# Kernel optimization log

Hardware: AMD Instinct MI355X
Metric: run time of the kernel (lower is better)

The kernel has to match this reference:

```python
import jax, jax.numpy as jnp
import numpy as np

B, T, D = 2, 2048, 1024
H, HS = 16, 64  # n_head, head_size; H*HS == D
THETA = 10000.0


def setup_inputs() -> dict:
    key = jax.random.key(0)
    ks = jax.random.split(key, 10)
    s = 0.02
    return {
        "x": jax.random.normal(ks[0], (B, T, D), jnp.float32),
        "attention_mask": jnp.ones((B, T), jnp.int32),
        # weights stored [in, out] (transposed torch Linear weight)
        "Wq": jax.random.normal(ks[1], (D, H * HS), jnp.float32) * s,
        "bq": jax.random.normal(ks[2], (H * HS,), jnp.float32) * s,
        "Wk": jax.random.normal(ks[3], (D, H * HS), jnp.float32) * s,
        "bk": jax.random.normal(ks[4], (H * HS,), jnp.float32) * s,
        "Wv": jax.random.normal(ks[5], (D, H * HS), jnp.float32) * s,
        "bv": jax.random.normal(ks[6], (H * HS,), jnp.float32) * s,
        "Wo": jax.random.normal(ks[7], (H * HS, D), jnp.float32) * s,
        "bo": jax.random.normal(ks[8], (D,), jnp.float32) * s,
    }


def _rotate_half(x):
    x1, x2 = x[..., : HS // 2], x[..., HS // 2:]
    return jnp.concatenate((-x2, x1), axis=-1)


def _rope_tables(seq_len, dtype):
    inv_freq = 1.0 / (THETA ** (jnp.arange(0, HS, 2, dtype=jnp.float32) / HS))
    t = jnp.arange(seq_len, dtype=jnp.float32)
    freqs = t[:, None] * inv_freq[None, :]            # [T, HS/2]
    emb = jnp.concatenate((freqs, freqs), axis=-1)    # [T, HS]
    return jnp.cos(emb).astype(dtype), jnp.sin(emb).astype(dtype)


def attention_fwd(x, attention_mask, Wq, bq, Wk, bk, Wv, bv, Wo, bo):
    b, t, c = x.shape
    # QKV projections -> [B, H, T, HS]
    q = (x @ Wq + bq).reshape(b, t, H, HS).transpose(0, 2, 1, 3)
    k = (x @ Wk + bk).reshape(b, t, H, HS).transpose(0, 2, 1, 3)
    v = (x @ Wv + bv).reshape(b, t, H, HS).transpose(0, 2, 1, 3)
    # rotary embedding
    cos, sin = _rope_tables(t, x.dtype)               # [T, HS]
    q = q * cos + _rotate_half(q) * sin
    k = k * cos + _rotate_half(k) * sin
    # expanded causal+padding mask: mask[:,None,None,:] expanded to [B,1,T,T] then tril
    causal = jnp.tril(jnp.ones((t, t), dtype=bool))
    keep = (attention_mask[:, None, None, :] != 0) & causal[None, None]  # [B,1,T,T]
    scale = 1.0 / np.sqrt(HS)
    scores = jnp.einsum('bhqd,bhkd->bhqk', q, k) * scale
    scores = jnp.where(keep, scores, jnp.finfo(scores.dtype).min)
    att = jax.nn.softmax(scores, axis=-1)
    y = jnp.einsum('bhqk,bhkd->bhqd', att, v)         # [B,H,T,HS]
    y = y.transpose(0, 2, 1, 3).reshape(b, t, H * HS)
    return y @ Wo + bo


def reference(x, attention_mask, Wq, bq, Wk, bk, Wv, bv, Wo, bo):
    return attention_fwd(x, attention_mask, Wq, bq, Wk, bk, Wv, bv, Wo, bo)
```

## Files before the change

kernel.cpp:

```cpp
#include <hip/hip_runtime.h>

#define T_SEQ 2048
#define NB 2
#define NH 16
#define HS 64
#define DMODEL 1024
#define NEG_BIG (-3.0e38f)
#define FIXED_M 16.0f

typedef __attribute__((ext_vector_type(8))) short bf16x8;
typedef __attribute__((ext_vector_type(4))) float f32x4;
#define MFMA16 __builtin_amdgcn_mfma_f32_16x16x32_bf16

__device__ __forceinline__ float bfu2f(unsigned int u) {
    union { unsigned int i; float f; } z; z.i = u << 16; return z.f;
}
__device__ __forceinline__ unsigned short f2bfu(float f) {
    union { float f; unsigned int i; } z; z.f = f;
    unsigned int x = z.i;
    unsigned int r = x + 0x7fffu + ((x >> 16) & 1u);
    return (unsigned short)(r >> 16);
}
__device__ __forceinline__ unsigned int pack_bf16(float a, float b) {
    union { float f; unsigned int u; } x, y; x.f = a; y.f = b;
    return __builtin_amdgcn_perm(y.u + 0x8000u, x.u + 0x8000u, 0x07060302u);
}
__device__ __forceinline__ void gl2lds16(const unsigned short* g, unsigned short* l) {
    __builtin_amdgcn_global_load_lds(
        (const __attribute__((address_space(1))) unsigned int*)g,
        (__attribute__((address_space(3))) unsigned int*)l, 16, 0, 0);
}

__global__ __launch_bounds__(256) void prep_kernel(
    const float4* __restrict__ x4, ushort4* __restrict__ o4,
    const float* __restrict__ W0, const float* __restrict__ W1,
    const float* __restrict__ W2, const float* __restrict__ W3,
    unsigned short* __restrict__ T0, unsigned short* __restrict__ T1,
    unsigned short* __restrict__ T2, unsigned short* __restrict__ T3)
{
    const int t = threadIdx.x;
    if (blockIdx.z < 4) {
        __shared__ float tile[32][33];
        const float* W = (blockIdx.z == 0) ? W0 : (blockIdx.z == 1) ? W1 : (blockIdx.z == 2) ? W2 : W3;
        unsigned short* T = (blockIdx.z == 0) ? T0 : (blockIdx.z == 1) ? T1 : (blockIdx.z == 2) ? T2 : T3;
        const int k0 = blockIdx.x * 32, n0 = blockIdx.y * 32;
        const int r = t >> 5, c = t & 31;
        #pragma unroll
        for (int i = 0; i < 4; ++i)
            tile[r + 8 * i][c] = W[(size_t)(k0 + r + 8 * i) * DMODEL + n0 + c];
        __syncthreads();
        #pragma unroll
        for (int i = 0; i < 4; ++i)
            T[(size_t)(n0 + r + 8 * i) * DMODEL + k0 + c] = f2bfu(tile[c][r + 8 * i]);
    } else {
        const int n4 = NB * T_SEQ * DMODEL / 4;
        for (int i = (blockIdx.y * 32 + blockIdx.x) * 256 + t; i < n4; i += 32 * 32 * 256) {
            float4 f = x4[i];
            ushort4 u;
            u.x = f2bfu(f.x); u.y = f2bfu(f.y); u.z = f2bfu(f.z); u.w = f2bfu(f.w);
            o4[i] = u;
        }
    }
}

__global__ __launch_bounds__(256) void qkv_mfma_kernel(
    const unsigned short* __restrict__ A,
    const unsigned short* __restrict__ Wqt, const unsigned short* __restrict__ Wkt,
    const unsigned short* __restrict__ Wvt,
    const float* __restrict__ bq, const float* __restrict__ bk, const float* __restrict__ bv,
    unsigned short* __restrict__ qo, unsigned short* __restrict__ ko,
    unsigned short* __restrict__ vt)
{
    __shared__ unsigned short As[64 * 64];
    __shared__ unsigned short Bs[128 * 64];
    const int tid = threadIdx.x;
    const int wave = tid >> 6, lane = tid & 63;
    const int lane15 = lane & 15, quad = lane >> 4;
    const int sw = lane15 & 7;
    const int z = blockIdx.z;
    const unsigned short* Bt = (z == 0) ? Wqt : (z == 1) ? Wkt : Wvt;
    const float* bias = (z == 0) ? bq : (z == 1) ? bk : bv;
    const int m0 = blockIdx.x * 64, n0 = blockIdx.y * 128;
    const int mh = (wave & 1) * 32, nh = (wave >> 1) * 64;
    const int oks0 = ((0 + quad) ^ sw) * 8;
    const int oks1 = ((4 + quad) ^ sw) * 8;

    f32x4 acc[2][4];
    #pragma unroll
    for (int i = 0; i < 2; ++i)
        #pragma unroll
        for (int j = 0; j < 4; ++j) acc[i][j] = (f32x4){0.f, 0.f, 0.f, 0.f};

    int srow[4], soff[4];
    #pragma unroll
    for (int it = 0; it < 4; ++it) {
        int cc = it * 256 + tid;
        srow[it] = cc >> 3;
        soff[it] = ((cc & 7) ^ (srow[it] & 7)) * 8;
    }

    for (int kk = 0; kk < 16; ++kk) {
        __syncthreads();
        #pragma unroll
        for (int it = 0; it < 2; ++it) {
            int cc = it * 256 + tid;
            gl2lds16(A + (size_t)(m0 + srow[it]) * DMODEL + kk * 64 + soff[it], As + cc * 8);
        }
        #pragma unroll
        for (int it = 0; it < 4; ++it) {
            int cc = it * 256 + tid;
            gl2lds16(Bt + (size_t)(n0 + srow[it]) * DMODEL + kk * 64 + soff[it], Bs + cc * 8);
        }
        __syncthreads();
        #pragma unroll
        for (int ks = 0; ks < 2; ++ks) {
            const int o = ks ? oks1 : oks0;
            bf16x8 af[2], bfr[4];
            #pragma unroll
            for (int i = 0; i < 2; ++i)
                af[i] = *(const bf16x8*)(As + (mh + i * 16 + lane15) * 64 + o);
            #pragma unroll
            for (int j = 0; j < 4; ++j)
                bfr[j] = *(const bf16x8*)(Bs + (nh + j * 16 + lane15) * 64 + o);
            #pragma unroll
            for (int i = 0; i < 2; ++i)
                #pragma unroll
                for (int j = 0; j < 4; ++j)
                    acc[i][j] = MFMA16(af[i], bfr[j], acc[i][j], 0, 0, 0);
        }
    }

    const int n0c = n0 + nh;
    const int head = n0c >> 6;
    const float bj0 = bias[n0c + lane15];
    const float bj1 = bias[n0c + 16 + lane15];
    const float bj2 = bias[n0c + 32 + lane15];
    const float bj3 = bias[n0c + 48 + lane15];

    if (z < 2) {
        unsigned short* outp = (z == 0) ? qo : ko;
        const float osc = (z == 0) ? 0.18033688011112042f : 1.0f;
        const float inv0 = __builtin_exp2f(-(float)(lane15)      * 0.41524101186092029f);
        const float inv1 = __builtin_exp2f(-(float)(lane15 + 16) * 0.41524101186092029f);
        #pragma unroll
        for (int i = 0; i < 2; ++i) {
            #pragma unroll
            for (int r = 0; r < 4; ++r) {
                int tok = m0 + mh + i * 16 + quad * 4 + r;
                int bb = tok >> 11, t = tok & (T_SEQ - 1);
                float a0 = (float)t * inv0, a1 = (float)t * inv1;
                float sn0, cs0, sn1, cs1;
                __sincosf(a0, &sn0, &cs0);
                __sincosf(a1, &sn1, &cs1);
                float v0 = acc[i][0][r] + bj0, v1 = acc[i][1][r] + bj1;
                float v2 = acc[i][2][r] + bj2, v3 = acc[i][3][r] + bj3;
                size_t base = ((size_t)(bb * NH + head) * T_SEQ + t) * HS;
                outp[base + lane15]      = f2bfu((v0 * cs0 - v2 * sn0) * osc);
                outp[base + 16 + lane15] = f2bfu((v1 * cs1 - v3 * sn1) * osc);
                outp[base + 32 + lane15] = f2bfu((v2 * cs0 + v0 * sn0) * osc);
                outp[base + 48 + lane15] = f2bfu((v3 * cs1 + v1 * sn1) * osc);
            }
        }
    } else {
        #pragma unroll
        for (int i = 0; i < 2; ++i) {
            int tok0_ = m0 + mh + i * 16 + quad * 4;
            int bb = tok0_ >> 11, t0 = tok0_ & (T_SEQ - 1);
            #pragma unroll
            for (int j = 0; j < 4; ++j) {
                float bj = (j == 0) ? bj0 : (j == 1) ? bj1 : (j == 2) ? bj2 : bj3;
                ushort4 u;
                u.x = f2bfu(acc[i][j][0] + bj);
                u.y = f2bfu(acc[i][j][1] + bj);
                u.z = f2bfu(acc[i][j][2] + bj);
                u.w = f2bfu(acc[i][j][3] + bj);
                *(ushort4*)(vt + ((size_t)(bb * NH + head) * HS + j * 16 + lane15) * T_SEQ + t0) = u;
            }
        }
    }
}

__global__ __launch_bounds__(128, 2) void attn_mfma_kernel(
    const unsigned short* __restrict__ q,
    const unsigned short* __restrict__ k,
    const unsigned short* __restrict__ vt,
    const int* __restrict__ mask,
    unsigned short* __restrict__ pO,
    float* __restrict__ pl)
{
    __shared__ unsigned short Ks[64 * 64];
    __shared__ unsigned short Vs[64 * 64];
    __shared__ unsigned short Pt[2][32 * 64];
    const int tid = threadIdx.x;
    const int wave = tid >> 6, lane = tid & 63;
    const int lane15 = lane & 15, quad = lane >> 4;
    const int sw = lane15 & 7;
    const int oks0 = ((0 + quad) ^ sw) * 8;
    const int oks1 = ((4 + quad) ^ sw) * 8;
    const int bid = blockIdx.x;
    const int bh = bid & 31;
    const int u = 79 - (bid >> 5);
    int qB, c;
    if (u < 8)       { qB = u;                 c = 0; }
    else if (u < 24) { int t = u - 8;  qB = 8  + (t >> 1); c = t & 1; }
    else if (u < 48) { int t = u - 24; qB = 16 + t / 3;    c = t % 3; }
    else             { int t = u - 48; qB = 24 + (t >> 2); c = t & 3; }
    const int slot = bh * 80 + u;
    const int nc  = (qB + 8) >> 3;
    const int len = (qB + nc) / nc;
    const int kt0 = c * len;
    const int kt1 = (kt0 + len - 1 < qB) ? kt0 + len - 1 : qB;
    const int b = bh >> 4;
    const int q0 = qB * 64 + wave * 32;

    const unsigned short* kbase = k  + (size_t)bh * T_SEQ * HS;
    const unsigned short* vbase = vt + (size_t)bh * HS * T_SEQ;

    bf16x8 qf[2][2];
    #pragma unroll
    for (int g = 0; g < 2; ++g) {
        const unsigned short* qrow = q + ((size_t)bh * T_SEQ + q0 + g * 16 + lane15) * HS;
        qf[g][0] = *(const bf16x8*)(qrow + quad * 8);
        qf[g][1] = *(const bf16x8*)(qrow + 32 + quad * 8);
    }

    f32x4 accO[2][4];
    #pragma unroll
    for (int g = 0; g < 2; ++g)
        #pragma unroll
        for (int dt = 0; dt < 4; ++dt) accO[g][dt] = (f32x4){0.f, 0.f, 0.f, 0.f};
    float l_part[2] = {0.f, 0.f};

    int srow[4], soff[4];
    #pragma unroll
    for (int it = 0; it < 4; ++it) {
        int cc = it * 128 + tid;
        srow[it] = cc >> 3;
        soff[it] = ((cc & 7) ^ (srow[it] & 7)) * 8;
    }

    for (int kt = kt0; kt <= kt1; ++kt) {
        const int k0 = kt * 64;
        __syncthreads();
        #pragma unroll
        for (int it = 0; it < 4; ++it) {
            int cc = it * 128 + tid;
            gl2lds16(kbase + (size_t)(k0 + srow[it]) * HS + soff[it], Ks + cc * 8);
            gl2lds16(vbase + (size_t)srow[it] * T_SEQ + k0 + soff[it], Vs + cc * 8);
        }
        unsigned long long bal = __ballot(mask[b * T_SEQ + k0 + lane] != 0);
        __syncthreads();

        f32x4 s[2][4];
        #pragma unroll
        for (int jt = 0; jt < 4; ++jt) {
            bf16x8 kf0 = *(const bf16x8*)(Ks + (jt * 16 + lane15) * 64 + oks0);
            bf16x8 kf1 = *(const bf16x8*)(Ks + (jt * 16 + lane15) * 64 + oks1);
            #pragma unroll
            for (int g = 0; g < 2; ++g) {
                f32x4 t_ = (f32x4){0.f, 0.f, 0.f, 0.f};
                t_ = MFMA16(kf0, qf[g][0], t_, 0, 0, 0);
                t_ = MFMA16(kf1, qf[g][1], t_, 0, 0, 0);
                s[g][jt] = t_;
            }
        }

        const bool need_mask = (k0 + 63 > q0) || (bal != ~0ull);
        if (need_mask) {
            #pragma unroll
            for (int g = 0; g < 2; ++g) {
                const int qpos = q0 + g * 16 + lane15;
                #pragma unroll
                for (int jt = 0; jt < 4; ++jt) {
                    unsigned int mnib = (unsigned int)(bal >> (jt * 16 + quad * 4)) & 15u;
                    #pragma unroll
                    for (int r = 0; r < 4; ++r) {
                        int kpos = k0 + jt * 16 + quad * 4 + r;
                        bool ok = (kpos <= qpos) && ((mnib >> r) & 1u);
                        s[g][jt][r] = ok ? s[g][jt][r] : NEG_BIG;
                    }
                }
            }
        }
        #pragma unroll
        for (int g = 0; g < 2; ++g)
            #pragma unroll
            for (int jt = 0; jt < 4; ++jt)
                #pragma unroll
                for (int r = 0; r < 4; ++r) {
                    float p = exp2f(s[g][jt][r] - FIXED_M);
                    s[g][jt][r] = p;
                    l_part[g] += p;
                }

        #pragma unroll
        for (int g = 0; g < 2; ++g)
            #pragma unroll
            for (int jt = 0; jt < 4; ++jt) {
                unsigned int p01 = pack_bf16(s[g][jt][0], s[g][jt][1]);
                unsigned int p23 = pack_bf16(s[g][jt][2], s[g][jt][3]);
                int pchunk = (2 * jt + (quad >> 1)) ^ sw;
                int paddr = (g * 16 + lane15) * 64 + pchunk * 8 + (quad & 1) * 4;
                *(uint2*)(&Pt[wave][paddr]) = make_uint2(p01, p23);
            }

        bf16x8 pf[2][2];
        #pragma unroll
        for (int g = 0; g < 2; ++g) {
            pf[g][0] = *(const bf16x8*)(&Pt[wave][(g * 16 + lane15) * 64 + oks0]);
            pf[g][1] = *(const bf16x8*)(&Pt[wave][(g * 16 + lane15) * 64 + oks1]);
        }
        #pragma unroll
        for (int dt = 0; dt < 4; ++dt) {
            bf16x8 vf0 = *(const bf16x8*)(Vs + (dt * 16 + lane15) * 64 + oks0);
            bf16x8 vf1 = *(const bf16x8*)(Vs + (dt * 16 + lane15) * 64 + oks1);
            #pragma unroll
            for (int g = 0; g < 2; ++g) {
                accO[g][dt] = MFMA16(pf[g][0], vf0, accO[g][dt], 0, 0, 0);
                accO[g][dt] = MFMA16(pf[g][1], vf1, accO[g][dt], 0, 0, 0);
            }
        }
    }

    unsigned short* ob = pO + (size_t)slot * 4096;
    #pragma unroll
    for (int g = 0; g < 2; ++g)
        #pragma unroll
        for (int r = 0; r < 4; ++r) {
            int row = wave * 32 + g * 16 + quad * 4 + r;
            #pragma unroll
            for (int dt = 0; dt < 4; ++dt)
                ob[row * 64 + dt * 16 + lane15] = f2bfu(accO[g][dt][r]);
        }
    #pragma unroll
    for (int g = 0; g < 2; ++g) {
        float l = l_part[g];
        l += __shfl_xor(l, 16);
        l += __shfl_xor(l, 32);
        if (quad == 0)
            pl[slot * 64 + wave * 32 + g * 16 + lane15] = l;
    }
}

__global__ __launch_bounds__(256) void attn_combine_kernel(
    const unsigned short* __restrict__ pO, const float* __restrict__ pl,
    unsigned short* __restrict__ y)
{
    const int qB = blockIdx.x, bh = blockIdx.y;
    const int b = bh >> 4, h = bh & 15;
    const int tid = threadIdx.x;
    const int row = tid >> 2, cb = (tid & 3) * 16;
    const int nch = (qB + 8) >> 3;
    const int p = (qB < 8) ? qB : (qB < 16) ? 8 + 2 * (qB - 8)
               : (qB < 24) ? 24 + 3 * (qB - 16) : 48 + 4 * (qB - 24);
    const int slot0 = bh * 80 + p;

    float L = 0.f;
    for (int ch = 0; ch < nch; ++ch) L += pl[(slot0 + ch) * 64 + row];
    const float invL = 1.0f / L;

    float a[16];
    #pragma unroll
    for (int i = 0; i < 16; ++i) a[i] = 0.f;
    for (int ch = 0; ch < nch; ++ch) {
        const unsigned short* o = pO + (size_t)(slot0 + ch) * 4096 + row * 64 + cb;
        #pragma unroll
        for (int j = 0; j < 4; ++j) {
            ushort4 u = *(const ushort4*)(o + j * 4);
            a[j * 4 + 0] += bfu2f(u.x); a[j * 4 + 1] += bfu2f(u.y);
            a[j * 4 + 2] += bfu2f(u.z); a[j * 4 + 3] += bfu2f(u.w);
        }
    }
    unsigned short* yrow = y + (size_t)(b * T_SEQ + qB * 64 + row) * DMODEL + h * HS + cb;
    #pragma unroll
    for (int j = 0; j < 4; ++j) {
        ushort4 o;
        o.x = f2bfu(a[j * 4 + 0] * invL); o.y = f2bfu(a[j * 4 + 1] * invL);
        o.z = f2bfu(a[j * 4 + 2] * invL); o.w = f2bfu(a[j * 4 + 3] * invL);
        *(ushort4*)(yrow + j * 4) = o;
    }
}

__global__ __launch_bounds__(256) void outproj_mfma_kernel(
    const unsigned short* __restrict__ A,
    const unsigned short* __restrict__ Bt,
    const float* __restrict__ bo, float* __restrict__ out)
{
    __shared__ unsigned short As[64 * 64];
    __shared__ unsigned short Bs[128 * 64];
    const int tid = threadIdx.x;
    const int wave = tid >> 6, lane = tid & 63;
    const int lane15 = lane & 15, quad = lane >> 4;
    const int sw = lane15 & 7;
    const int oks0 = ((0 + quad) ^ sw) * 8;
    const int oks1 = ((4 + quad) ^ sw) * 8;
    const int m0 = blockIdx.x * 64, n0 = blockIdx.y * 128;
    const int mh = (wave & 1) * 32, nh = (wave >> 1) * 64;

    f32x4 acc[2][4];
    #pragma unroll
    for (int i = 0; i < 2; ++i)
        #pragma unroll
        for (int j = 0; j < 4; ++j) acc[i][j] = (f32x4){0.f, 0.f, 0.f, 0.f};

    int srow[4], soff[4];
    #pragma unroll
    for (int it = 0; it < 4; ++it) {
        int cc = it * 256 + tid;
        srow[it] = cc >> 3;
        soff[it] = ((cc & 7) ^ (srow[it] & 7)) * 8;
    }

    for (int kk = 0; kk < 16; ++kk) {
        __syncthreads();
        #pragma unroll
        for (int it = 0; it < 2; ++it) {
            int cc = it * 256 + tid;
            gl2lds16(A + (size_t)(m0 + srow[it]) * DMODEL + kk * 64 + soff[it], As + cc * 8);
        }
        #pragma unroll
        for (int it = 0; it < 4; ++it) {
            int cc = it * 256 + tid;
            gl2lds16(Bt + (size_t)(n0 + srow[it]) * DMODEL + kk * 64 + soff[it], Bs + cc * 8);
        }
        __syncthreads();
        #pragma unroll
        for (int ks = 0; ks < 2; ++ks) {
            const int o = ks ? oks1 : oks0;
            bf16x8 af[2], bfr[4];
            #pragma unroll
            for (int i = 0; i < 2; ++i)
                af[i] = *(const bf16x8*)(As + (mh + i * 16 + lane15) * 64 + o);
            #pragma unroll
            for (int j = 0; j < 4; ++j)
                bfr[j] = *(const bf16x8*)(Bs + (nh + j * 16 + lane15) * 64 + o);
            #pragma unroll
            for (int i = 0; i < 2; ++i)
                #pragma unroll
                for (int j = 0; j < 4; ++j)
                    acc[i][j] = MFMA16(af[i], bfr[j], acc[i][j], 0, 0, 0);
        }
    }

    const int n0c = n0 + nh;
    const float bj0 = bo[n0c + lane15];
    const float bj1 = bo[n0c + 16 + lane15];
    const float bj2 = bo[n0c + 32 + lane15];
    const float bj3 = bo[n0c + 48 + lane15];
    #pragma unroll
    for (int i = 0; i < 2; ++i) {
        #pragma unroll
        for (int r = 0; r < 4; ++r) {
            int tok = m0 + mh + i * 16 + quad * 4 + r;
            float* orow = out + (size_t)tok * DMODEL + n0c;
            orow[lane15]      = acc[i][0][r] + bj0;
            orow[16 + lane15] = acc[i][1][r] + bj1;
            orow[32 + lane15] = acc[i][2][r] + bj2;
            orow[48 + lane15] = acc[i][3][r] + bj3;
        }
    }
}

extern "C" void kernel_launch(void* const* d_in, const int* in_sizes, int n_in,
                              void* d_out, int out_size, void* d_ws, size_t ws_size,
                              hipStream_t stream)
{
    const float* x  = (const float*)d_in[0];
    const int* mask = (const int*)d_in[1];
    const float* Wq = (const float*)d_in[2];
    const float* bq = (const float*)d_in[3];
    const float* Wk = (const float*)d_in[4];
    const float* bk = (const float*)d_in[5];
    const float* Wv = (const float*)d_in[6];
    const float* bv = (const float*)d_in[7];
    const float* Wo = (const float*)d_in[8];
    const float* bo = (const float*)d_in[9];

    unsigned short* ws = (unsigned short*)d_ws;
    const size_t M1 = 1024 * 1024;
    unsigned short* qw  = ws;
    unsigned short* kw  = ws + 4 * M1;
    unsigned short* vtw = ws + 8 * M1;
    unsigned short* yw  = ws + 12 * M1;
    unsigned short* Wot = ws + 16 * M1;
    unsigned short* xb  = ws + 17 * M1;
    unsigned short* Wqt = ws + 21 * M1;
    unsigned short* Wkt = ws + 22 * M1;
    unsigned short* Wvt = ws + 23 * M1;
    unsigned short* pO  = ws + 17 * M1;
    float* pl = (float*)(ws + 27 * M1);

    prep_kernel<<<dim3(32, 32, 5), 256, 0, stream>>>(
        (const float4*)x, (ushort4*)xb, Wq, Wk, Wv, Wo, Wqt, Wkt, Wvt, Wot);
    qkv_mfma_kernel<<<dim3(64, 8, 3), 256, 0, stream>>>(
        xb, Wqt, Wkt, Wvt, bq, bk, bv, qw, kw, vtw);
    attn_mfma_kernel<<<2560, 128, 0, stream>>>(
        qw, kw, vtw, mask, pO, pl);
    attn_combine_kernel<<<dim3(32, 32), 256, 0, stream>>>(
        pO, pl, yw);
    outproj_mfma_kernel<<<dim3(64, 8), 256, 0, stream>>>(
        yw, Wot, bo, (float*)d_out);
}
```

Before: 188.1 us.

## Prefetch next K/V tile into registers and compute row sums with MFMA

Replaces the direct global-to-LDS async copies with a register double buffer. The next K/V tile and its mask values are loaded into registers while the current tile is computed, then written to LDS at the start of the next iteration, so global load latency overlaps with compute. The softmax denominator is now computed by an extra MFMA of the bf16 P tile against a ones vector instead of scalar adds and shuffles, and the fixed max offset subtraction before exp2 is dropped. This raises register pressure, and removing the offset risks overflow unless the scores are already offset elsewhere.

```diff
diff --git a/kernel.cpp b/kernel.cpp
--- a/kernel.cpp
+++ b/kernel.cpp
@@ -6,7 +6,6 @@
 #define HS 64
 #define DMODEL 1024
 #define NEG_BIG (-3.0e38f)
-#define FIXED_M 16.0f
 
 typedef __attribute__((ext_vector_type(8))) short bf16x8;
 typedef __attribute__((ext_vector_type(4))) float f32x4;
@@ -216,6 +215,22 @@
     const unsigned short* kbase = k  + (size_t)bh * T_SEQ * HS;
     const unsigned short* vbase = vt + (size_t)bh * HS * T_SEQ;
 
+    int srow[4], soff[4];
+    #pragma unroll
+    for (int it = 0; it < 4; ++it) {
+        int cc = it * 128 + tid;
+        srow[it] = cc >> 3;
+        soff[it] = ((cc & 7) ^ (srow[it] & 7)) * 8;
+    }
+
+    int mv = mask[b * T_SEQ + kt0 * 64 + lane];
+    uint4 kreg[4], vreg[4];
+    #pragma unroll
+    for (int it = 0; it < 4; ++it) {
+        kreg[it] = *(const uint4*)(kbase + (size_t)(kt0 * 64 + srow[it]) * HS + soff[it]);
+        vreg[it] = *(const uint4*)(vbase + (size_t)srow[it] * T_SEQ + kt0 * 64 + soff[it]);
+    }
+
     bf16x8 qf[2][2];
     #pragma unroll
     for (int g = 0; g < 2; ++g) {
@@ -224,20 +239,18 @@
         qf[g][1] = *(const bf16x8*)(qrow + 32 + quad * 8);
     }
 
+    bf16x8 ones;
+    #pragma unroll
+    for (int i = 0; i < 8; ++i) ones[i] = (short)0x3F80;
+
     f32x4 accO[2][4];
     #pragma unroll
     for (int g = 0; g < 2; ++g)
         #pragma unroll
         for (int dt = 0; dt < 4; ++dt) accO[g][dt] = (f32x4){0.f, 0.f, 0.f, 0.f};
-    float l_part[2] = {0.f, 0.f};
-
-    int srow[4], soff[4];
-    #pragma unroll
-    for (int it = 0; it < 4; ++it) {
-        int cc = it * 128 + tid;
-        srow[it] = cc >> 3;
-        soff[it] = ((cc & 7) ^ (srow[it] & 7)) * 8;
-    }
+    f32x4 acc_l[2];
+    acc_l[0] = (f32x4){0.f, 0.f, 0.f, 0.f};
+    acc_l[1] = (f32x4){0.f, 0.f, 0.f, 0.f};
 
     for (int kt = kt0; kt <= kt1; ++kt) {
         const int k0 = kt * 64;
@@ -245,10 +258,19 @@
         #pragma unroll
         for (int it = 0; it < 4; ++it) {
             int cc = it * 128 + tid;
-            gl2lds16(kbase + (size_t)(k0 + srow[it]) * HS + soff[it], Ks + cc * 8);
-            gl2lds16(vbase + (size_t)srow[it] * T_SEQ + k0 + soff[it], Vs + cc * 8);
-        }
-        unsigned long long bal = __ballot(mask[b * T_SEQ + k0 + lane] != 0);
+            *(uint4*)(Ks + cc * 8) = kreg[it];
+            *(uint4*)(Vs + cc * 8) = vreg[it];
+        }
+        unsigned long long bal = __ballot(mv != 0);
+        if (kt < kt1) {
+            const int kn = k0 + 64;
+            mv = mask[b * T_SEQ + kn + lane];
+            #pragma unroll
+            for (int it = 0; it < 4; ++it) {
+                kreg[it] = *(const uint4*)(kbase + (size_t)(kn + srow[it]) * HS + soff[it]);
+                vreg[it] = *(const uint4*)(vbase + (size_t)srow[it] * T_SEQ + kn + soff[it]);
+            }
+        }
         __syncthreads();
 
         f32x4 s[2][4];
@@ -287,11 +309,8 @@
             #pragma unroll
             for (int jt = 0; jt < 4; ++jt)
                 #pragma unroll
-                for (int r = 0; r < 4; ++r) {
-                    float p = exp2f(s[g][jt][r] - FIXED_M);
-                    s[g][jt][r] = p;
-                    l_part[g] += p;
-                }
+                for (int r = 0; r < 4; ++r)
+                    s[g][jt][r] = exp2f(s[g][jt][r]);
 
         #pragma unroll
         for (int g = 0; g < 2; ++g)
@@ -320,6 +339,11 @@
                 accO[g][dt] = MFMA16(pf[g][1], vf1, accO[g][dt], 0, 0, 0);
             }
         }
+        #pragma unroll
+        for (int g = 0; g < 2; ++g) {
+            acc_l[g] = MFMA16(pf[g][0], ones, acc_l[g], 0, 0, 0);
+            acc_l[g] = MFMA16(pf[g][1], ones, acc_l[g], 0, 0, 0);
+        }
     }
 
     unsigned short* ob = pO + (size_t)slot * 4096;
@@ -332,13 +356,12 @@
             for (int dt = 0; dt < 4; ++dt)
                 ob[row * 64 + dt * 16 + lane15] = f2bfu(accO[g][dt][r]);
         }
-    #pragma unroll
-    for (int g = 0; g < 2; ++g) {
-        float l = l_part[g];
-        l += __shfl_xor(l, 16);
-        l += __shfl_xor(l, 32);
-        if (quad == 0)
-            pl[slot * 64 + wave * 32 + g * 16 + lane15] = l;
+    if (lane15 == 0) {
+        #pragma unroll
+        for (int g = 0; g < 2; ++g)
+            #pragma unroll
+            for (int r = 0; r < 4; ++r)
+                pl[slot * 64 + wave * 32 + g * 16 + quad * 4 + r] = acc_l[g][r];
     }
 }
 
```

After: 241.5 us. 28.3% more time.

## Split attention block into four 16-row waves and compute row sums via MFMA

Applied to the files above, without the earlier changes.

The attention kernel now runs 256 threads per block, with each of four waves handling 16 query rows instead of two waves handling 32. This roughly halves per-wave register state and doubles the waves that share each K/V tile. Row sums of P are now computed with an extra MFMA against a vector of ones instead of scalar adds and shuffles. The fixed max offset of 16 is dropped from exp2, which changes numerical behaviour and could overflow for large scores. It also gives up the reuse of K/V fragments across two row groups within a wave.

```diff
diff --git a/kernel.cpp b/kernel.cpp
--- a/kernel.cpp
+++ b/kernel.cpp
@@ -6,7 +6,6 @@
 #define HS 64
 #define DMODEL 1024
 #define NEG_BIG (-3.0e38f)
-#define FIXED_M 16.0f
 
 typedef __attribute__((ext_vector_type(8))) short bf16x8;
 typedef __attribute__((ext_vector_type(4))) float f32x4;
@@ -180,7 +179,7 @@
     }
 }
 
-__global__ __launch_bounds__(128, 2) void attn_mfma_kernel(
+__global__ __launch_bounds__(256, 2) void attn_mfma_kernel(
     const unsigned short* __restrict__ q,
     const unsigned short* __restrict__ k,
     const unsigned short* __restrict__ vt,
@@ -190,7 +189,7 @@
 {
     __shared__ unsigned short Ks[64 * 64];
     __shared__ unsigned short Vs[64 * 64];
-    __shared__ unsigned short Pt[2][32 * 64];
+    __shared__ unsigned short Pt[4][16 * 64];
     const int tid = threadIdx.x;
     const int wave = tid >> 6, lane = tid & 63;
     const int lane15 = lane & 15, quad = lane >> 4;
@@ -211,30 +210,31 @@
     const int kt0 = c * len;
     const int kt1 = (kt0 + len - 1 < qB) ? kt0 + len - 1 : qB;
     const int b = bh >> 4;
-    const int q0 = qB * 64 + wave * 32;
+    const int q0w = qB * 64 + wave * 16;
 
     const unsigned short* kbase = k  + (size_t)bh * T_SEQ * HS;
     const unsigned short* vbase = vt + (size_t)bh * HS * T_SEQ;
 
-    bf16x8 qf[2][2];
-    #pragma unroll
-    for (int g = 0; g < 2; ++g) {
-        const unsigned short* qrow = q + ((size_t)bh * T_SEQ + q0 + g * 16 + lane15) * HS;
-        qf[g][0] = *(const bf16x8*)(qrow + quad * 8);
-        qf[g][1] = *(const bf16x8*)(qrow + 32 + quad * 8);
-    }
-
-    f32x4 accO[2][4];
-    #pragma unroll
-    for (int g = 0; g < 2; ++g)
-        #pragma unroll
-        for (int dt = 0; dt < 4; ++dt) accO[g][dt] = (f32x4){0.f, 0.f, 0.f, 0.f};
-    float l_part[2] = {0.f, 0.f};
-
-    int srow[4], soff[4];
-    #pragma unroll
-    for (int it = 0; it < 4; ++it) {
-        int cc = it * 128 + tid;
+    bf16x8 qf0, qf1;
+    {
+        const unsigned short* qrow = q + ((size_t)bh * T_SEQ + q0w + lane15) * HS;
+        qf0 = *(const bf16x8*)(qrow + quad * 8);
+        qf1 = *(const bf16x8*)(qrow + 32 + quad * 8);
+    }
+
+    bf16x8 ones;
+    #pragma unroll
+    for (int i = 0; i < 8; ++i) ones[i] = (short)0x3F80;
+
+    f32x4 accO[4];
+    #pragma unroll
+    for (int dt = 0; dt < 4; ++dt) accO[dt] = (f32x4){0.f, 0.f, 0.f, 0.f};
+    f32x4 acc_l = (f32x4){0.f, 0.f, 0.f, 0.f};
+
+    int srow[2], soff[2];
+    #pragma unroll
+    for (int it = 0; it < 2; ++it) {
+        int cc = it * 256 + tid;
         srow[it] = cc >> 3;
         soff[it] = ((cc & 7) ^ (srow[it] & 7)) * 8;
     }
@@ -243,102 +243,79 @@
         const int k0 = kt * 64;
         __syncthreads();
         #pragma unroll
-        for (int it = 0; it < 4; ++it) {
-            int cc = it * 128 + tid;
+        for (int it = 0; it < 2; ++it) {
+            int cc = it * 256 + tid;
             gl2lds16(kbase + (size_t)(k0 + srow[it]) * HS + soff[it], Ks + cc * 8);
             gl2lds16(vbase + (size_t)srow[it] * T_SEQ + k0 + soff[it], Vs + cc * 8);
         }
         unsigned long long bal = __ballot(mask[b * T_SEQ + k0 + lane] != 0);
         __syncthreads();
 
-        f32x4 s[2][4];
+        f32x4 s[4];
         #pragma unroll
         for (int jt = 0; jt < 4; ++jt) {
             bf16x8 kf0 = *(const bf16x8*)(Ks + (jt * 16 + lane15) * 64 + oks0);
             bf16x8 kf1 = *(const bf16x8*)(Ks + (jt * 16 + lane15) * 64 + oks1);
-            #pragma unroll
-            for (int g = 0; g < 2; ++g) {
-                f32x4 t_ = (f32x4){0.f, 0.f, 0.f, 0.f};
-                t_ = MFMA16(kf0, qf[g][0], t_, 0, 0, 0);
-                t_ = MFMA16(kf1, qf[g][1], t_, 0, 0, 0);
-                s[g][jt] = t_;
-            }
-        }
-
-        const bool need_mask = (k0 + 63 > q0) || (bal != ~0ull);
+            f32x4 t_ = (f32x4){0.f, 0.f, 0.f, 0.f};
+            t_ = MFMA16(kf0, qf0, t_, 0, 0, 0);
+            t_ = MFMA16(kf1, qf1, t_, 0, 0, 0);
+            s[jt] = t_;
+        }
+
+        const bool need_mask = (k0 + 63 > q0w) || (bal != ~0ull);
         if (need_mask) {
-            #pragma unroll
-            for (int g = 0; g < 2; ++g) {
-                const int qpos = q0 + g * 16 + lane15;
+            const int qpos = q0w + lane15;
+            #pragma unroll
+            for (int jt = 0; jt < 4; ++jt) {
+                unsigned int mnib = (unsigned int)(bal >> (jt * 16 + quad * 4)) & 15u;
                 #pragma unroll
-                for (int jt = 0; jt < 4; ++jt) {
-                    unsigned int mnib = (unsigned int)(bal >> (jt * 16 + quad * 4)) & 15u;
-                    #pragma unroll
-                    for (int r = 0; r < 4; ++r) {
-                        int kpos = k0 + jt * 16 + quad * 4 + r;
-                        bool ok = (kpos <= qpos) && ((mnib >> r) & 1u);
-                        s[g][jt][r] = ok ? s[g][jt][r] : NEG_BIG;
-                    }
+                for (int r = 0; r < 4; ++r) {
+                    int kpos = k0 + jt * 16 + quad * 4 + r;
+                    bool ok = (kpos <= qpos) && ((mnib >> r) & 1u);
+                    s[jt][r] = ok ? s[jt][r] : NEG_BIG;
                 }
             }
         }
         #pragma unroll
-        for (int g = 0; g < 2; ++g)
-            #pragma unroll
-            for (int jt = 0; jt < 4; ++jt)
-                #pragma unroll
-                for (int r = 0; r < 4; ++r) {
-                    float p = exp2f(s[g][jt][r] - FIXED_M);
-                    s[g][jt][r] = p;
-                    l_part[g] += p;
-                }
-
-        #pragma unroll
-        for (int g = 0; g < 2; ++g)
-            #pragma unroll
-            for (int jt = 0; jt < 4; ++jt) {
-                unsigned int p01 = pack_bf16(s[g][jt][0], s[g][jt][1]);
-                unsigned int p23 = pack_bf16(s[g][jt][2], s[g][jt][3]);
-                int pchunk = (2 * jt + (quad >> 1)) ^ sw;
-                int paddr = (g * 16 + lane15) * 64 + pchunk * 8 + (quad & 1) * 4;
-                *(uint2*)(&Pt[wave][paddr]) = make_uint2(p01, p23);
-            }
-
-        bf16x8 pf[2][2];
-        #pragma unroll
-        for (int g = 0; g < 2; ++g) {
-            pf[g][0] = *(const bf16x8*)(&Pt[wave][(g * 16 + lane15) * 64 + oks0]);
-            pf[g][1] = *(const bf16x8*)(&Pt[wave][(g * 16 + lane15) * 64 + oks1]);
-        }
+        for (int jt = 0; jt < 4; ++jt)
+            #pragma unroll
+            for (int r = 0; r < 4; ++r)
+                s[jt][r] = exp2f(s[jt][r]);
+
+        #pragma unroll
+        for (int jt = 0; jt < 4; ++jt) {
+            unsigned int p01 = pack_bf16(s[jt][0], s[jt][1]);
+            unsigned int p23 = pack_bf16(s[jt][2], s[jt][3]);
+            int pchunk = (2 * jt + (quad >> 1)) ^ sw;
+            int paddr = lane15 * 64 + pchunk * 8 + (quad & 1) * 4;
+            *(uint2*)(&Pt[wave][paddr]) = make_uint2(p01, p23);
+        }
+
+        bf16x8 pf0 = *(const bf16x8*)(&Pt[wave][lane15 * 64 + oks0]);
+        bf16x8 pf1 = *(const bf16x8*)(&Pt[wave][lane15 * 64 + oks1]);
         #pragma unroll
         for (int dt = 0; dt < 4; ++dt) {
             bf16x8 vf0 = *(const bf16x8*)(Vs + (dt * 16 + lane15) * 64 + oks0);
             bf16x8 vf1 = *(const bf16x8*)(Vs + (dt * 16 + lane15) * 64 + oks1);
-            #pragma unroll
-            for (int g = 0; g < 2; ++g) {
-                accO[g][dt] = MFMA16(pf[g][0], vf0, accO[g][dt], 0, 0, 0);
-                accO[g][dt] = MFMA16(pf[g][1], vf1, accO[g][dt], 0, 0, 0);
-            }
-        }
+            accO[dt] = MFMA16(pf0, vf0, accO[dt], 0, 0, 0);
+            accO[dt] = MFMA16(pf1, vf1, accO[dt], 0, 0, 0);
+        }
+        acc_l = MFMA16(pf0, ones, acc_l, 0, 0, 0);
+        acc_l = MFMA16(pf1, ones, acc_l, 0, 0, 0);
     }
 
     unsigned short* ob = pO + (size_t)slot * 4096;
     #pragma unroll
-    for (int g = 0; g < 2; ++g)
-        #pragma unroll
-        for (int r = 0; r < 4; ++r) {
-            int row = wave * 32 + g * 16 + quad * 4 + r;
-            #pragma unroll
-            for (int dt = 0; dt < 4; ++dt)
-                ob[row * 64 + dt * 16 + lane15] = f2bfu(accO[g][dt][r]);
-        }
-    #pragma unroll
-    for (int g = 0; g < 2; ++g) {
-        float l = l_part[g];
-        l += __shfl_xor(l, 16);
-        l += __shfl_xor(l, 32);
-        if (quad == 0)
-            pl[slot * 64 + wave * 32 + g * 16 + lane15] = l;
+    for (int r = 0; r < 4; ++r) {
+        int row = wave * 16 + quad * 4 + r;
+        #pragma unroll
+        for (int dt = 0; dt < 4; ++dt)
+            ob[row * 64 + dt * 16 + lane15] = f2bfu(accO[dt][r]);
+    }
+    if (lane15 == 0) {
+        #pragma unroll
+        for (int r = 0; r < 4; ++r)
+            pl[slot * 64 + wave * 16 + quad * 4 + r] = acc_l[r];
     }
 }
 
@@ -494,7 +471,7 @@
         (const float4*)x, (ushort4*)xb, Wq, Wk, Wv, Wo, Wqt, Wkt, Wvt, Wot);
     qkv_mfma_kernel<<<dim3(64, 8, 3), 256, 0, stream>>>(
         xb, Wqt, Wkt, Wvt, bq, bk, bv, qw, kw, vtw);
-    attn_mfma_kernel<<<2560, 128, 0, stream>>>(
+    attn_mfma_kernel<<<2560, 256, 0, stream>>>(
         qw, kw, vtw, mask, pO, pl);
     attn_combine_kernel<<<dim3(32, 32), 256, 0, stream>>>(
         pO, pl, yw);
```

New measurement: 184.5 us. Within noise of the previous version (-1.9%).
